# Kernel tuning notes

Measured on AMD Instinct MI355X. Metric: run time of the kernel, lower is better.

## Reference

```python
import jax, jax.numpy as jnp
import numpy as np

N, E, F_IN, HID, HEADS, NCLASS, NGRAPH = 50000, 600000, 128, 64, 2, 10, 64
NEG_SLOPE = 0.2


def _gat_conv(x, src, dst, W, a_src, a_dst, b):
    # x: [N, Fin]; W: [Fin, H*C]; a_src/a_dst: [H, C]; b: [H*C]
    n = x.shape[0]
    h = (x @ W).reshape(n, HEADS, -1)              # [N, H, C]
    alpha_src = (h * a_src).sum(-1)                # [N, H]
    alpha_dst = (h * a_dst).sum(-1)                # [N, H]
    e = jax.nn.leaky_relu(alpha_src[src] + alpha_dst[dst], NEG_SLOPE)  # [E, H]
    # segment softmax over destination nodes (every node has a self-loop)
    m = jax.ops.segment_max(e, dst, num_segments=n)
    e = jnp.exp(e - m[dst])
    denom = jax.ops.segment_sum(e, dst, num_segments=n)
    alpha = e / (denom[dst] + 1e-16)               # [E, H]
    msg = h[src] * alpha[:, :, None]               # [E, H, C]
    out = jax.ops.segment_sum(msg, dst, num_segments=n)  # [N, H, C]
    return out.reshape(n, -1) + b


def setup_inputs() -> dict:
    key = jax.random.key(0)
    ks = jax.random.split(key, 16)
    HC = HID * HEADS
    inp = {
        "x": jax.random.normal(ks[0], (N, F_IN), dtype=jnp.float32),
        "edge_index": jax.random.randint(ks[1], (2, E), 0, N, dtype=jnp.int32),
        "batch": jnp.sort(jax.random.randint(ks[2], (N,), 0, NGRAPH, dtype=jnp.int32)),
    }
    dims = [F_IN, HC, HC]  # conv0, conv1, conv_last input widths
    for i, din in enumerate(dims):
        inp[f"W{i}"] = jax.random.normal(ks[3 + 4 * i], (din, HC), dtype=jnp.float32) * (1.0 / np.sqrt(din))
        inp[f"a_src{i}"] = jax.random.normal(ks[4 + 4 * i], (HEADS, HID), dtype=jnp.float32) * 0.1
        inp[f"a_dst{i}"] = jax.random.normal(ks[5 + 4 * i], (HEADS, HID), dtype=jnp.float32) * 0.1
        inp[f"b{i}"] = jnp.zeros((HC,), dtype=jnp.float32)
    inp["lin_w"] = jax.random.normal(ks[15], (HC, NCLASS), dtype=jnp.float32) * (1.0 / np.sqrt(HC))
    inp["lin_b"] = jnp.zeros((NCLASS,), dtype=jnp.float32)
    return inp


def reference(x, edge_index, batch, W0, a_src0, a_dst0, b0, W1, a_src1, a_dst1, b1,
              W2, a_src2, a_dst2, b2, lin_w, lin_b):
    n = x.shape[0]
    loops = jnp.arange(n, dtype=edge_index.dtype)
    src = jnp.concatenate([edge_index[0], loops])  # add_self_loops=True in PyG GATConv
    dst = jnp.concatenate([edge_index[1], loops])
    # eval mode: dropout is identity; use_bn=False so LayerNorms are skipped
    h = _gat_conv(x, src, dst, W0, a_src0, a_dst0, b0)
    h = jax.nn.elu(h)
    h = _gat_conv(h, src, dst, W1, a_src1, a_dst1, b1)
    h = jax.nn.elu(h)
    h = _gat_conv(h, src, dst, W2, a_src2, a_dst2, b2)
    # global mean pool over graphs
    sums = jax.ops.segment_sum(h, batch, num_segments=NGRAPH)
    counts = jax.ops.segment_sum(jnp.ones((n,), h.dtype), batch, num_segments=NGRAPH)
    pooled = sums / jnp.maximum(counts, 1.0)[:, None]
    logits = pooled @ lin_w + lin_b
    return jax.nn.softmax(logits, axis=1)
```

## Files before the change

### kernel.cpp

```cpp
#include <hip/hip_runtime.h>

#define NN 50000
#define EE 600000
#define ET 650000
#define NGRAPH 64
#define NCLASS 10
#define NEG 0.2f

typedef unsigned short u16;
typedef __attribute__((ext_vector_type(8))) short short8;
typedef __attribute__((ext_vector_type(4))) float f32x4;

__device__ __forceinline__ float bf2f(u16 u) {
  union { float f; unsigned int i; } v; v.i = ((unsigned int)u) << 16; return v.f;
}
__device__ __forceinline__ u16 f2bf(float f) {
  union { float f; unsigned int i; } v; v.f = f;
  unsigned int r = v.i + 0x7FFFu + ((v.i >> 16) & 1u);
  return (u16)(r >> 16);
}
__device__ __forceinline__ float lrelu(float x) { return x >= 0.f ? x : NEG * x; }
__device__ __forceinline__ float plo(unsigned p) {
  union { float f; unsigned int i; } v; v.i = p << 16; return v.f;
}
__device__ __forceinline__ float phi(unsigned p) {
  union { float f; unsigned int i; } v; v.i = p & 0xffff0000u; return v.f;
}

__global__ __launch_bounds__(256) void detect_k(const void* __restrict__ x, int* __restrict__ flag) {
  __shared__ int sc[256];
  const float* xf = (const float*)x;
  int t = threadIdx.x, c = 0;
  for (int i = 0; i < 4; ++i) {
    float a = fabsf(xf[t * 4 + i]);
    if (a > 1e-4f && a < 100.f) c++;
  }
  sc[t] = c;
  __syncthreads();
  for (int o = 128; o > 0; o >>= 1) { if (t < o) sc[t] += sc[t + o]; __syncthreads(); }
  if (t == 0) flag[0] = (sc[0] >= 512) ? 1 : 0;
}

__global__ __launch_bounds__(256) void conv_x_k(const void* __restrict__ x, u16* __restrict__ xc,
                                                const int* __restrict__ flag) {
  int i = (blockIdx.x * 256 + threadIdx.x) * 4;
  if (i >= NN * 128) return;
  if (flag[0]) {
    const float* s = (const float*)x + i;
    xc[i] = f2bf(s[0]); xc[i + 1] = f2bf(s[1]); xc[i + 2] = f2bf(s[2]); xc[i + 3] = f2bf(s[3]);
  } else {
    *(uint2*)(xc + i) = *(const uint2*)((const u16*)x + i);
  }
}

__global__ __launch_bounds__(256) void conv_w_k(const void* __restrict__ w0, const void* __restrict__ w1,
                                                const void* __restrict__ w2, u16* __restrict__ wc,
                                                const int* __restrict__ flag) {
  int idx = blockIdx.x * 256 + threadIdx.x;
  const void* s = (idx >> 14) == 0 ? w0 : ((idx >> 14) == 1 ? w1 : w2);
  int l = idx & 16383;
  wc[idx] = flag[0] ? f2bf(((const float*)s)[l]) : ((const u16*)s)[l];
}

__global__ __launch_bounds__(256) void conv_p_k(const void* as0, const void* ad0, const void* b0,
                                                const void* as1, const void* ad1, const void* b1,
                                                const void* as2, const void* ad2, const void* b2,
                                                const void* lw, const void* lb,
                                                float* __restrict__ pf, const int* __restrict__ flag) {
  const void* srcs[11] = {as0, ad0, b0, as1, ad1, b1, as2, ad2, b2, lw, lb};
  const int offs[12] = {0, 128, 256, 384, 512, 640, 768, 896, 1024, 1152, 2432, 2442};
  int f = flag[0];
  for (int idx = threadIdx.x; idx < 2442; idx += 256) {
    int k = 0;
    while (idx >= offs[k + 1]) k++;
    int l = idx - offs[k];
    pf[idx] = f ? ((const float*)srcs[k])[l] : bf2f(((const u16*)srcs[k])[l]);
  }
}

__global__ __launch_bounds__(256) void init_k(int* counts, int* fill, int* roff, float* psum) {
  int i = blockIdx.x * 256 + threadIdx.x;
  if (i < NN) { counts[i] = 1; fill[i] = 0; }
  if (i < NGRAPH * 128) psum[i] = 0.f;
  if (i == 0) roff[NN] = ET;
}

__global__ __launch_bounds__(256) void count_k(const int* __restrict__ ei, int* __restrict__ counts) {
  int e = blockIdx.x * 256 + threadIdx.x;
  if (e < EE) atomicAdd(&counts[ei[EE + e]], 1);
}

__global__ __launch_bounds__(256) void scan_a(const int* __restrict__ counts, int* __restrict__ part) {
  __shared__ int s[256];
  int t = threadIdx.x, i = blockIdx.x * 256 + t;
  s[t] = (i < NN) ? counts[i] : 0;
  __syncthreads();
  for (int o = 128; o > 0; o >>= 1) { if (t < o) s[t] += s[t + o]; __syncthreads(); }
  if (t == 0) part[blockIdx.x] = s[0];
}

__global__ __launch_bounds__(256) void scan_b(int* part) {
  __shared__ int s[256];
  int t = threadIdx.x;
  int v = (t < 196) ? part[t] : 0;
  s[t] = v;
  __syncthreads();
  for (int o = 1; o < 256; o <<= 1) {
    int add = (t >= o) ? s[t - o] : 0;
    __syncthreads();
    s[t] += add;
    __syncthreads();
  }
  if (t < 196) part[t] = s[t] - v;
}

__global__ __launch_bounds__(256) void scan_c(const int* __restrict__ counts, const int* __restrict__ part,
                                              int* __restrict__ roff) {
  __shared__ int s[256];
  int t = threadIdx.x, i = blockIdx.x * 256 + t;
  int v = (i < NN) ? counts[i] : 0;
  s[t] = v;
  __syncthreads();
  for (int o = 1; o < 256; o <<= 1) {
    int add = (t >= o) ? s[t - o] : 0;
    __syncthreads();
    s[t] += add;
    __syncthreads();
  }
  if (i < NN) roff[i] = part[blockIdx.x] + s[t] - v;
}

__global__ __launch_bounds__(256) void fill_k(const int* __restrict__ ei, const int* __restrict__ roff,
                                              int* __restrict__ fill, int* __restrict__ csr) {
  int i = blockIdx.x * 256 + threadIdx.x;
  if (i >= ET) return;
  int s, d;
  if (i < EE) { s = ei[i]; d = ei[EE + i]; } else { s = d = i - EE; }
  int pos = roff[d] + atomicAdd(&fill[d], 1);
  if ((unsigned)pos < (unsigned)ET) csr[pos] = s;
}

__global__ __launch_bounds__(256) void gemm_k(const u16* __restrict__ A, const u16* __restrict__ Wg,
                                              const float* __restrict__ a_src, const float* __restrict__ a_dst,
                                              unsigned* __restrict__ h2, float* __restrict__ al_s,
                                              float* __restrict__ al_d) {
  __shared__ u16 lds[128 * 128];
  int tid = threadIdx.x;
  for (int idx = tid; idx < 128 * 128; idx += 256) {
    int k = idx >> 7, c = idx & 127;
    int slot = (k >> 3) ^ (c & 15);
    lds[c * 128 + slot * 8 + (k & 7)] = Wg[idx];
  }
  __syncthreads();
  int wid = tid >> 6, lane = tid & 63;
  int l15 = lane & 15, quad = lane >> 4;
  int row0 = blockIdx.x * 64 + wid * 16;
  f32x4 acc[8];
#pragma unroll
  for (int t = 0; t < 8; ++t) { acc[t][0] = 0.f; acc[t][1] = 0.f; acc[t][2] = 0.f; acc[t][3] = 0.f; }
  int arow = row0 + l15;
  if (arow >= NN) arow = NN - 1;
#pragma unroll
  for (int ks = 0; ks < 4; ++ks) {
    short8 a = *(const short8*)(A + (size_t)arow * 128 + ks * 32 + quad * 8);
#pragma unroll
    for (int t = 0; t < 8; ++t) {
      int col = t * 16 + l15;
      int slot = (ks * 4 + quad) ^ l15;
      short8 b = *(const short8*)(&lds[col * 128 + slot * 8]);
      acc[t] = __builtin_amdgcn_mfma_f32_16x16x32_bf16(a, b, acc[t], 0, 0, 0);
    }
  }
  float vs[8], vd[8];
#pragma unroll
  for (int t = 0; t < 8; ++t) { vs[t] = a_src[t * 16 + l15]; vd[t] = a_dst[t * 16 + l15]; }
#pragma unroll
  for (int r = 0; r < 4; ++r) {
    int row = row0 + quad * 4 + r;
#pragma unroll
    for (int t = 0; t < 4; ++t) {
      if (row < NN) {
        unsigned lo = f2bf(acc[t][r]);
        unsigned hiv = f2bf(acc[t + 4][r]);
        h2[(size_t)row * 64 + t * 16 + l15] = lo | (hiv << 16);
      }
    }
    float s0 = 0.f, s1 = 0.f, d0 = 0.f, d1 = 0.f;
#pragma unroll
    for (int t = 0; t < 4; ++t) { s0 += acc[t][r] * vs[t]; d0 += acc[t][r] * vd[t]; }
#pragma unroll
    for (int t = 4; t < 8; ++t) { s1 += acc[t][r] * vs[t]; d1 += acc[t][r] * vd[t]; }
#pragma unroll
    for (int o = 1; o < 16; o <<= 1) {
      s0 += __shfl_xor(s0, o); s1 += __shfl_xor(s1, o);
      d0 += __shfl_xor(d0, o); d1 += __shfl_xor(d1, o);
    }
    if (row < NN && l15 == 0) {
      al_s[2 * row] = s0; al_s[2 * row + 1] = s1;
      al_d[2 * row] = d0; al_d[2 * row + 1] = d1;
    }
  }
}

__global__ __launch_bounds__(256) void agg_k(const unsigned* __restrict__ h2, const float* __restrict__ al_s,
                                             const float* __restrict__ al_d, const int* __restrict__ roff,
                                             const int* __restrict__ csr, const float* __restrict__ bias,
                                             u16* __restrict__ oB, float* __restrict__ psum,
                                             const int* __restrict__ batch, int last) {
  int wid = threadIdx.x >> 6, lane = threadIdx.x & 63;
  int n = blockIdx.x * 4 + wid;
  if (n >= NN) return;
  int base = roff[n], deg = roff[n + 1] - base;
  float ad0 = al_d[2 * n], ad1 = al_d[2 * n + 1];
  float acc0 = 0.f, acc1 = 0.f, den0, den1;

  if (deg <= 64) {
    int sv = 0;
    float e0 = -1e30f, e1 = -1e30f;
    if (lane < deg) {
      sv = csr[base + lane];
      float as0 = al_s[2 * sv], as1 = al_s[2 * sv + 1];
      e0 = lrelu(as0 + ad0); e1 = lrelu(as1 + ad1);
    }
    float m0 = e0, m1 = e1;
#pragma unroll
    for (int o = 32; o > 0; o >>= 1) { m0 = fmaxf(m0, __shfl_xor(m0, o)); m1 = fmaxf(m1, __shfl_xor(m1, o)); }
    float w0 = (lane < deg) ? __expf(e0 - m0) : 0.f;
    float w1 = (lane < deg) ? __expf(e1 - m1) : 0.f;
    den0 = w0; den1 = w1;
#pragma unroll
    for (int o = 32; o > 0; o >>= 1) { den0 += __shfl_xor(den0, o); den1 += __shfl_xor(den1, o); }
    int j = 0;
    for (; j + 4 <= deg; j += 4) {
      int s0 = __shfl(sv, j), s1 = __shfl(sv, j + 1), s2 = __shfl(sv, j + 2), s3 = __shfl(sv, j + 3);
      unsigned p0 = h2[(size_t)s0 * 64 + lane];
      unsigned p1 = h2[(size_t)s1 * 64 + lane];
      unsigned p2 = h2[(size_t)s2 * 64 + lane];
      unsigned p3 = h2[(size_t)s3 * 64 + lane];
      float a0 = __shfl(w0, j), a1 = __shfl(w0, j + 1), a2 = __shfl(w0, j + 2), a3 = __shfl(w0, j + 3);
      float b0 = __shfl(w1, j), b1 = __shfl(w1, j + 1), b2 = __shfl(w1, j + 2), b3 = __shfl(w1, j + 3);
      acc0 += a0 * plo(p0); acc1 += b0 * phi(p0);
      acc0 += a1 * plo(p1); acc1 += b1 * phi(p1);
      acc0 += a2 * plo(p2); acc1 += b2 * phi(p2);
      acc0 += a3 * plo(p3); acc1 += b3 * phi(p3);
    }
    for (; j < deg; ++j) {
      int sj = __shfl(sv, j);
      unsigned p = h2[(size_t)sj * 64 + lane];
      acc0 += __shfl(w0, j) * plo(p);
      acc1 += __shfl(w1, j) * phi(p);
    }
  } else {
    float m0 = -1e30f, m1 = -1e30f;
    for (int i = lane; i < deg; i += 64) {
      int s = csr[base + i];
      m0 = fmaxf(m0, lrelu(al_s[2 * s] + ad0));
      m1 = fmaxf(m1, lrelu(al_s[2 * s + 1] + ad1));
    }
#pragma unroll
    for (int o = 32; o > 0; o >>= 1) { m0 = fmaxf(m0, __shfl_xor(m0, o)); m1 = fmaxf(m1, __shfl_xor(m1, o)); }
    den0 = 0.f; den1 = 0.f;
    for (int c0 = 0; c0 < deg; c0 += 64) {
      int cnt = min(64, deg - c0);
      int sv = 0; float w0 = 0.f, w1 = 0.f;
      if (lane < cnt) {
        sv = csr[base + c0 + lane];
        w0 = __expf(lrelu(al_s[2 * sv] + ad0) - m0);
        w1 = __expf(lrelu(al_s[2 * sv + 1] + ad1) - m1);
      }
      for (int j = 0; j < cnt; ++j) {
        int sj = __shfl(sv, j);
        unsigned p = h2[(size_t)sj * 64 + lane];
        float w0j = __shfl(w0, j), w1j = __shfl(w1, j);
        acc0 += w0j * plo(p); acc1 += w1j * phi(p);
        den0 += w0j; den1 += w1j;
      }
    }
  }

  float v0 = acc0 / (den0 + 1e-16f) + bias[lane];
  float v1 = acc1 / (den1 + 1e-16f) + bias[64 + lane];
  if (last) {
    int g = batch[n]; if ((unsigned)g >= (unsigned)NGRAPH) g = 0;
    atomicAdd(&psum[g * 128 + lane], v0);
    atomicAdd(&psum[g * 128 + 64 + lane], v1);
  } else {
    v0 = v0 > 0.f ? v0 : __expf(v0) - 1.f;
    v1 = v1 > 0.f ? v1 : __expf(v1) - 1.f;
    oB[(size_t)n * 128 + lane] = f2bf(v0);
    oB[(size_t)n * 128 + 64 + lane] = f2bf(v1);
  }
}

__device__ __forceinline__ int lbound(const int* a, int n, int v) {
  int lo = 0, hi = n;
  while (lo < hi) { int mid = (lo + hi) >> 1; if (a[mid] < v) lo = mid + 1; else hi = mid; }
  return lo;
}

__global__ __launch_bounds__(128) void final_k(const float* __restrict__ psum, const int* __restrict__ batch,
                                               const float* __restrict__ lw, const float* __restrict__ lb,
                                               float* __restrict__ out) {
  __shared__ float p[128];
  __shared__ float lg[NCLASS];
  int g = blockIdx.x, t = threadIdx.x;
  int cnt = lbound(batch, NN, g + 1) - lbound(batch, NN, g);
  p[t] = psum[g * 128 + t] / fmaxf((float)cnt, 1.f);
  __syncthreads();
  if (t < NCLASS) {
    float acc = lb[t];
    for (int c = 0; c < 128; ++c) acc += p[c] * lw[c * NCLASS + t];
    lg[t] = acc;
  }
  __syncthreads();
  if (t < NCLASS) {
    float m = -1e30f;
    for (int j = 0; j < NCLASS; ++j) m = fmaxf(m, lg[j]);
    float sum = 0.f;
    for (int j = 0; j < NCLASS; ++j) sum += __expf(lg[j] - m);
    out[g * NCLASS + t] = __expf(lg[t] - m) / sum;
  }
}

extern "C" void kernel_launch(void* const* d_in, const int* in_sizes, int n_in,
                              void* d_out, int out_size, void* d_ws, size_t ws_size,
                              hipStream_t stream) {
  const void* x = d_in[0];
  const int* ei = (const int*)d_in[1];
  const int* batch = (const int*)d_in[2];
  float* out = (float*)d_out;

  size_t off = 0;
  auto alloc = [&](size_t bytes) -> void* {
    void* p = (char*)d_ws + off;
    off += (bytes + 255) & ~(size_t)255;
    return p;
  };
  int* flag = (int*)alloc(256);
  u16* xc = (u16*)alloc((size_t)NN * 128 * 2);
  u16* wc = (u16*)alloc((size_t)3 * 16384 * 2);
  float* pf = (float*)alloc(2442 * 4);
  unsigned* h2 = (unsigned*)alloc((size_t)NN * 64 * 4);
  u16* xb = (u16*)alloc((size_t)NN * 128 * 2);
  float* al_s = (float*)alloc((size_t)NN * 2 * 4);
  float* al_d = (float*)alloc((size_t)NN * 2 * 4);
  int* counts = (int*)alloc((size_t)NN * 4);
  int* fillc = (int*)alloc((size_t)NN * 4);
  int* roff = (int*)alloc((size_t)(NN + 1) * 4);
  int* csr = (int*)alloc((size_t)ET * 4);
  int* part = (int*)alloc(256 * 4);
  float* psum = (float*)alloc((size_t)NGRAPH * 128 * 4);

  detect_k<<<1, 256, 0, stream>>>(x, flag);
  conv_x_k<<<6250, 256, 0, stream>>>(x, xc, flag);
  conv_w_k<<<192, 256, 0, stream>>>(d_in[3], d_in[7], d_in[11], wc, flag);
  conv_p_k<<<1, 256, 0, stream>>>(d_in[4], d_in[5], d_in[6], d_in[8], d_in[9], d_in[10],
                                  d_in[12], d_in[13], d_in[14], d_in[15], d_in[16], pf, flag);

  init_k<<<196, 256, 0, stream>>>(counts, fillc, roff, psum);
  count_k<<<2344, 256, 0, stream>>>(ei, counts);
  scan_a<<<196, 256, 0, stream>>>(counts, part);
  scan_b<<<1, 256, 0, stream>>>(part);
  scan_c<<<196, 256, 0, stream>>>(counts, part, roff);
  fill_k<<<2540, 256, 0, stream>>>(ei, roff, fillc, csr);

  const u16* Ain = xc;
  for (int l = 0; l < 3; ++l) {
    gemm_k<<<782, 256, 0, stream>>>(Ain, wc + l * 16384, pf + l * 384, pf + l * 384 + 128,
                                    h2, al_s, al_d);
    agg_k<<<12500, 256, 0, stream>>>(h2, al_s, al_d, roff, csr, pf + l * 384 + 256,
                                     xb, psum, batch, l == 2);
    Ain = xb;
  }
  final_k<<<NGRAPH, 128, 0, stream>>>(psum, batch, pf + 1152, pf + 2432, out);
}
```

Baseline: 402.4 us.

## Precompute edge softmax weights with atomics and pack four nodes per wavefront

```diff
diff --git a/kernel.cpp b/kernel.cpp
--- a/kernel.cpp
+++ b/kernel.cpp
@@ -131,13 +131,14 @@
 }
 
 __global__ __launch_bounds__(256) void fill_k(const int* __restrict__ ei, const int* __restrict__ roff,
-                                              int* __restrict__ fill, int* __restrict__ csr) {
+                                              int* __restrict__ fill, int* __restrict__ csr,
+                                              int* __restrict__ edst) {
   int i = blockIdx.x * 256 + threadIdx.x;
   if (i >= ET) return;
   int s, d;
   if (i < EE) { s = ei[i]; d = ei[EE + i]; } else { s = d = i - EE; }
   int pos = roff[d] + atomicAdd(&fill[d], 1);
-  if ((unsigned)pos < (unsigned)ET) csr[pos] = s;
+  if ((unsigned)pos < (unsigned)ET) { csr[pos] = s; edst[pos] = d; }
 }
 
 __global__ __launch_bounds__(256) void gemm_k(const u16* __restrict__ A, const u16* __restrict__ Wg,
@@ -202,93 +203,87 @@
   }
 }
 
-__global__ __launch_bounds__(256) void agg_k(const unsigned* __restrict__ h2, const float* __restrict__ al_s,
-                                             const float* __restrict__ al_d, const int* __restrict__ roff,
+__global__ __launch_bounds__(256) void w_k(const float* __restrict__ al_s, const float* __restrict__ al_d,
+                                           const int* __restrict__ csr, const int* __restrict__ edst,
+                                           float* __restrict__ wbuf, float* __restrict__ den) {
+  int i = blockIdx.x * 256 + threadIdx.x;
+  if (i >= ET) return;
+  int s = csr[i], d = edst[i];
+  float w0 = __expf(lrelu(al_s[2 * s] + al_d[2 * d]));
+  float w1 = __expf(lrelu(al_s[2 * s + 1] + al_d[2 * d + 1]));
+  wbuf[2 * i] = w0;
+  wbuf[2 * i + 1] = w1;
+  atomicAdd(&den[2 * d], w0);
+  atomicAdd(&den[2 * d + 1], w1);
+}
+
+__global__ __launch_bounds__(256) void agg_k(const uint4* __restrict__ h2q, const float* __restrict__ wbuf,
+                                             const float* __restrict__ den, const int* __restrict__ roff,
                                              const int* __restrict__ csr, const float* __restrict__ bias,
                                              u16* __restrict__ oB, float* __restrict__ psum,
                                              const int* __restrict__ batch, int last) {
   int wid = threadIdx.x >> 6, lane = threadIdx.x & 63;
-  int n = blockIdx.x * 4 + wid;
-  if (n >= NN) return;
+  int li = lane & 15;
+  int n = blockIdx.x * 16 + wid * 4 + (lane >> 4);
+  if (n >= NN) n = NN - 1;
   int base = roff[n], deg = roff[n + 1] - base;
-  float ad0 = al_d[2 * n], ad1 = al_d[2 * n + 1];
-  float acc0 = 0.f, acc1 = 0.f, den0, den1;
-
-  if (deg <= 64) {
-    int sv = 0;
-    float e0 = -1e30f, e1 = -1e30f;
-    if (lane < deg) {
-      sv = csr[base + lane];
-      float as0 = al_s[2 * sv], as1 = al_s[2 * sv + 1];
-      e0 = lrelu(as0 + ad0); e1 = lrelu(as1 + ad1);
-    }
-    float m0 = e0, m1 = e1;
-#pragma unroll
-    for (int o = 32; o > 0; o >>= 1) { m0 = fmaxf(m0, __shfl_xor(m0, o)); m1 = fmaxf(m1, __shfl_xor(m1, o)); }
-    float w0 = (lane < deg) ? __expf(e0 - m0) : 0.f;
-    float w1 = (lane < deg) ? __expf(e1 - m1) : 0.f;
-    den0 = w0; den1 = w1;
-#pragma unroll
-    for (int o = 32; o > 0; o >>= 1) { den0 += __shfl_xor(den0, o); den1 += __shfl_xor(den1, o); }
-    int j = 0;
-    for (; j + 4 <= deg; j += 4) {
-      int s0 = __shfl(sv, j), s1 = __shfl(sv, j + 1), s2 = __shfl(sv, j + 2), s3 = __shfl(sv, j + 3);
-      unsigned p0 = h2[(size_t)s0 * 64 + lane];
-      unsigned p1 = h2[(size_t)s1 * 64 + lane];
-      unsigned p2 = h2[(size_t)s2 * 64 + lane];
-      unsigned p3 = h2[(size_t)s3 * 64 + lane];
-      float a0 = __shfl(w0, j), a1 = __shfl(w0, j + 1), a2 = __shfl(w0, j + 2), a3 = __shfl(w0, j + 3);
-      float b0 = __shfl(w1, j), b1 = __shfl(w1, j + 1), b2 = __shfl(w1, j + 2), b3 = __shfl(w1, j + 3);
-      acc0 += a0 * plo(p0); acc1 += b0 * phi(p0);
-      acc0 += a1 * plo(p1); acc1 += b1 * phi(p1);
-      acc0 += a2 * plo(p2); acc1 += b2 * phi(p2);
-      acc0 += a3 * plo(p3); acc1 += b3 * phi(p3);
-    }
-    for (; j < deg; ++j) {
-      int sj = __shfl(sv, j);
-      unsigned p = h2[(size_t)sj * 64 + lane];
-      acc0 += __shfl(w0, j) * plo(p);
-      acc1 += __shfl(w1, j) * phi(p);
+  int dm = deg;
+  dm = max(dm, __shfl_xor(dm, 16));
+  dm = max(dm, __shfl_xor(dm, 32));
+
+  float acc[8];
+#pragma unroll
+  for (int k = 0; k < 8; ++k) acc[k] = 0.f;
+
+  int sv = csr[base];
+  for (int j = 0; j < dm; ++j) {
+    int jn = j + 1; if (jn >= deg) jn = deg - 1;
+    int svn = csr[base + jn];
+    int jj = (j < deg) ? j : deg - 1;
+    float w0 = wbuf[2 * (base + jj)];
+    float w1 = wbuf[2 * (base + jj) + 1];
+    if (j >= deg) { w0 = 0.f; w1 = 0.f; }
+    uint4 p = h2q[(size_t)sv * 16 + li];
+    acc[0] += w0 * plo(p.x); acc[4] += w1 * phi(p.x);
+    acc[1] += w0 * plo(p.y); acc[5] += w1 * phi(p.y);
+    acc[2] += w0 * plo(p.z); acc[6] += w1 * phi(p.z);
+    acc[3] += w0 * plo(p.w); acc[7] += w1 * phi(p.w);
+    sv = svn;
+  }
+
+  float d0 = den[2 * n] + 1e-16f, d1 = den[2 * n + 1] + 1e-16f;
+  f32x4 b0 = *(const f32x4*)(bias + li * 4);
+  f32x4 b1 = *(const f32x4*)(bias + 64 + li * 4);
+  float v[8];
+#pragma unroll
+  for (int k = 0; k < 4; ++k) v[k] = acc[k] / d0 + b0[k];
+#pragma unroll
+  for (int k = 0; k < 4; ++k) v[4 + k] = acc[4 + k] / d1 + b1[k];
+
+  bool valid = (blockIdx.x * 16 + wid * 4 + (lane >> 4)) < NN;
+  if (last) {
+    if (valid) {
+      int g = batch[n]; if ((unsigned)g >= (unsigned)NGRAPH) g = 0;
+#pragma unroll
+      for (int k = 0; k < 4; ++k) atomicAdd(&psum[g * 128 + li * 4 + k], v[k]);
+#pragma unroll
+      for (int k = 0; k < 4; ++k) atomicAdd(&psum[g * 128 + 64 + li * 4 + k], v[4 + k]);
     }
   } else {
-    float m0 = -1e30f, m1 = -1e30f;
-    for (int i = lane; i < deg; i += 64) {
-      int s = csr[base + i];
-      m0 = fmaxf(m0, lrelu(al_s[2 * s] + ad0));
-      m1 = fmaxf(m1, lrelu(al_s[2 * s + 1] + ad1));
-    }
-#pragma unroll
-    for (int o = 32; o > 0; o >>= 1) { m0 = fmaxf(m0, __shfl_xor(m0, o)); m1 = fmaxf(m1, __shfl_xor(m1, o)); }
-    den0 = 0.f; den1 = 0.f;
-    for (int c0 = 0; c0 < deg; c0 += 64) {
-      int cnt = min(64, deg - c0);
-      int sv = 0; float w0 = 0.f, w1 = 0.f;
-      if (lane < cnt) {
-        sv = csr[base + c0 + lane];
-        w0 = __expf(lrelu(al_s[2 * sv] + ad0) - m0);
-        w1 = __expf(lrelu(al_s[2 * sv + 1] + ad1) - m1);
-      }
-      for (int j = 0; j < cnt; ++j) {
-        int sj = __shfl(sv, j);
-        unsigned p = h2[(size_t)sj * 64 + lane];
-        float w0j = __shfl(w0, j), w1j = __shfl(w1, j);
-        acc0 += w0j * plo(p); acc1 += w1j * phi(p);
-        den0 += w0j; den1 += w1j;
-      }
-    }
-  }
-
-  float v0 = acc0 / (den0 + 1e-16f) + bias[lane];
-  float v1 = acc1 / (den1 + 1e-16f) + bias[64 + lane];
-  if (last) {
-    int g = batch[n]; if ((unsigned)g >= (unsigned)NGRAPH) g = 0;
-    atomicAdd(&psum[g * 128 + lane], v0);
-    atomicAdd(&psum[g * 128 + 64 + lane], v1);
-  } else {
-    v0 = v0 > 0.f ? v0 : __expf(v0) - 1.f;
-    v1 = v1 > 0.f ? v1 : __expf(v1) - 1.f;
-    oB[(size_t)n * 128 + lane] = f2bf(v0);
-    oB[(size_t)n * 128 + 64 + lane] = f2bf(v1);
+    ushort4 lo, hi;
+    float e;
+    e = v[0]; lo.x = f2bf(e > 0.f ? e : __expf(e) - 1.f);
+    e = v[1]; lo.y = f2bf(e > 0.f ? e : __expf(e) - 1.f);
+    e = v[2]; lo.z = f2bf(e > 0.f ? e : __expf(e) - 1.f);
+    e = v[3]; lo.w = f2bf(e > 0.f ? e : __expf(e) - 1.f);
+    e = v[4]; hi.x = f2bf(e > 0.f ? e : __expf(e) - 1.f);
+    e = v[5]; hi.y = f2bf(e > 0.f ? e : __expf(e) - 1.f);
+    e = v[6]; hi.z = f2bf(e > 0.f ? e : __expf(e) - 1.f);
+    e = v[7]; hi.w = f2bf(e > 0.f ? e : __expf(e) - 1.f);
+    if (valid) {
+      *(ushort4*)(oB + (size_t)n * 128 + li * 4) = lo;
+      *(ushort4*)(oB + (size_t)n * 128 + 64 + li * 4) = hi;
+    }
   }
 }
 
@@ -348,6 +343,9 @@
   int* fillc = (int*)alloc((size_t)NN * 4);
   int* roff = (int*)alloc((size_t)(NN + 1) * 4);
   int* csr = (int*)alloc((size_t)ET * 4);
+  int* edst = (int*)alloc((size_t)ET * 4);
+  float* wbuf = (float*)alloc((size_t)ET * 2 * 4);
+  float* den = (float*)alloc((size_t)NN * 2 * 4);
   int* part = (int*)alloc(256 * 4);
   float* psum = (float*)alloc((size_t)NGRAPH * 128 * 4);
 
@@ -362,14 +360,16 @@
   scan_a<<<196, 256, 0, stream>>>(counts, part);
   scan_b<<<1, 256, 0, stream>>>(part);
   scan_c<<<196, 256, 0, stream>>>(counts, part, roff);
-  fill_k<<<2540, 256, 0, stream>>>(ei, roff, fillc, csr);
+  fill_k<<<2540, 256, 0, stream>>>(ei, roff, fillc, csr, edst);
 
   const u16* Ain = xc;
   for (int l = 0; l < 3; ++l) {
     gemm_k<<<782, 256, 0, stream>>>(Ain, wc + l * 16384, pf + l * 384, pf + l * 384 + 128,
                                     h2, al_s, al_d);
-    agg_k<<<12500, 256, 0, stream>>>(h2, al_s, al_d, roff, csr, pf + l * 384 + 256,
-                                     xb, psum, batch, l == 2);
+    hipMemsetAsync(den, 0, (size_t)NN * 2 * 4, stream);
+    w_k<<<2540, 256, 0, stream>>>(al_s, al_d, csr, edst, wbuf, den);
+    agg_k<<<3125, 256, 0, stream>>>((const uint4*)h2, wbuf, den, roff, csr, pf + l * 384 + 256,
+                                    xb, psum, batch, l == 2);
     Ain = xb;
   }
   final_k<<<NGRAPH, 128, 0, stream>>>(psum, batch, pf + 1152, pf + 2432, out);
```

After: 779.5 us. +93.7%, slower.

## Store aggregated features head-interleaved and permute weight rows to match; unroll gather by 8

Applied to the files above, without the earlier changes.

```diff
diff --git a/kernel.cpp b/kernel.cpp
--- a/kernel.cpp
+++ b/kernel.cpp
@@ -57,8 +57,11 @@
                                                 const void* __restrict__ w2, u16* __restrict__ wc,
                                                 const int* __restrict__ flag) {
   int idx = blockIdx.x * 256 + threadIdx.x;
-  const void* s = (idx >> 14) == 0 ? w0 : ((idx >> 14) == 1 ? w1 : w2);
-  int l = idx & 16383;
+  int layer = idx >> 14;
+  const void* s = layer == 0 ? w0 : (layer == 1 ? w1 : w2);
+  int r = (idx >> 7) & 127, ccol = idx & 127;
+  int sr = (layer == 0) ? r : ((r >> 1) + ((r & 1) << 6));
+  int l = sr * 128 + ccol;
   wc[idx] = flag[0] ? f2bf(((const float*)s)[l]) : ((const u16*)s)[l];
 }
 
@@ -205,11 +208,10 @@
 __global__ __launch_bounds__(256) void agg_k(const unsigned* __restrict__ h2, const float* __restrict__ al_s,
                                              const float* __restrict__ al_d, const int* __restrict__ roff,
                                              const int* __restrict__ csr, const float* __restrict__ bias,
-                                             u16* __restrict__ oB, float* __restrict__ psum,
+                                             unsigned* __restrict__ oB2, float* __restrict__ psum,
                                              const int* __restrict__ batch, int last) {
   int wid = threadIdx.x >> 6, lane = threadIdx.x & 63;
   int n = blockIdx.x * 4 + wid;
-  if (n >= NN) return;
   int base = roff[n], deg = roff[n + 1] - base;
   float ad0 = al_d[2 * n], ad1 = al_d[2 * n + 1];
   float acc0 = 0.f, acc1 = 0.f, den0, den1;
@@ -219,8 +221,8 @@
     float e0 = -1e30f, e1 = -1e30f;
     if (lane < deg) {
       sv = csr[base + lane];
-      float as0 = al_s[2 * sv], as1 = al_s[2 * sv + 1];
-      e0 = lrelu(as0 + ad0); e1 = lrelu(as1 + ad1);
+      e0 = lrelu(al_s[2 * sv] + ad0);
+      e1 = lrelu(al_s[2 * sv + 1] + ad1);
     }
     float m0 = e0, m1 = e1;
 #pragma unroll
@@ -231,18 +233,29 @@
 #pragma unroll
     for (int o = 32; o > 0; o >>= 1) { den0 += __shfl_xor(den0, o); den1 += __shfl_xor(den1, o); }
     int j = 0;
-    for (; j + 4 <= deg; j += 4) {
+    for (; j + 8 <= deg; j += 8) {
       int s0 = __shfl(sv, j), s1 = __shfl(sv, j + 1), s2 = __shfl(sv, j + 2), s3 = __shfl(sv, j + 3);
+      int s4 = __shfl(sv, j + 4), s5 = __shfl(sv, j + 5), s6 = __shfl(sv, j + 6), s7 = __shfl(sv, j + 7);
       unsigned p0 = h2[(size_t)s0 * 64 + lane];
       unsigned p1 = h2[(size_t)s1 * 64 + lane];
       unsigned p2 = h2[(size_t)s2 * 64 + lane];
       unsigned p3 = h2[(size_t)s3 * 64 + lane];
+      unsigned p4 = h2[(size_t)s4 * 64 + lane];
+      unsigned p5 = h2[(size_t)s5 * 64 + lane];
+      unsigned p6 = h2[(size_t)s6 * 64 + lane];
+      unsigned p7 = h2[(size_t)s7 * 64 + lane];
       float a0 = __shfl(w0, j), a1 = __shfl(w0, j + 1), a2 = __shfl(w0, j + 2), a3 = __shfl(w0, j + 3);
+      float a4 = __shfl(w0, j + 4), a5 = __shfl(w0, j + 5), a6 = __shfl(w0, j + 6), a7 = __shfl(w0, j + 7);
       float b0 = __shfl(w1, j), b1 = __shfl(w1, j + 1), b2 = __shfl(w1, j + 2), b3 = __shfl(w1, j + 3);
+      float b4 = __shfl(w1, j + 4), b5 = __shfl(w1, j + 5), b6 = __shfl(w1, j + 6), b7 = __shfl(w1, j + 7);
       acc0 += a0 * plo(p0); acc1 += b0 * phi(p0);
       acc0 += a1 * plo(p1); acc1 += b1 * phi(p1);
       acc0 += a2 * plo(p2); acc1 += b2 * phi(p2);
       acc0 += a3 * plo(p3); acc1 += b3 * phi(p3);
+      acc0 += a4 * plo(p4); acc1 += b4 * phi(p4);
+      acc0 += a5 * plo(p5); acc1 += b5 * phi(p5);
+      acc0 += a6 * plo(p6); acc1 += b6 * phi(p6);
+      acc0 += a7 * plo(p7); acc1 += b7 * phi(p7);
     }
     for (; j < deg; ++j) {
       int sj = __shfl(sv, j);
@@ -287,8 +300,8 @@
   } else {
     v0 = v0 > 0.f ? v0 : __expf(v0) - 1.f;
     v1 = v1 > 0.f ? v1 : __expf(v1) - 1.f;
-    oB[(size_t)n * 128 + lane] = f2bf(v0);
-    oB[(size_t)n * 128 + 64 + lane] = f2bf(v1);
+    unsigned lo = f2bf(v0), hi = f2bf(v1);
+    oB2[(size_t)n * 64 + lane] = lo | (hi << 16);
   }
 }
 
@@ -341,7 +354,7 @@
   u16* wc = (u16*)alloc((size_t)3 * 16384 * 2);
   float* pf = (float*)alloc(2442 * 4);
   unsigned* h2 = (unsigned*)alloc((size_t)NN * 64 * 4);
-  u16* xb = (u16*)alloc((size_t)NN * 128 * 2);
+  unsigned* xb = (unsigned*)alloc((size_t)NN * 64 * 4);
   float* al_s = (float*)alloc((size_t)NN * 2 * 4);
   float* al_d = (float*)alloc((size_t)NN * 2 * 4);
   int* counts = (int*)alloc((size_t)NN * 4);
@@ -370,7 +383,7 @@
                                     h2, al_s, al_d);
     agg_k<<<12500, 256, 0, stream>>>(h2, al_s, al_d, roff, csr, pf + l * 384 + 256,
                                      xb, psum, batch, l == 2);
-    Ain = xb;
+    Ain = (const u16*)xb;
   }
   final_k<<<NGRAPH, 128, 0, stream>>>(psum, batch, pf + 1152, pf + 2432, out);
 }
```

Measured after the change: 408.1 us. About the same (+1.4%).
